# Kernel optimization log

Measured on AMD Instinct MI355X. Metric: run time of the kernel, lower is better.

## Reference

```python
import jax, jax.numpy as jnp
import numpy as np

B, M, N, K = 64, 1024, 1024, 128

def setup_inputs() -> dict:
    key = jax.random.key(0)
    k1, k2, k3 = jax.random.split(key, 3)
    # int8 operands (stored as int32 per spec; values fit in int8 range)
    a = jax.random.randint(k1, (B, M, K), 0, 127, dtype=jnp.int32)
    b = jax.random.randint(k2, (B, N, K), 0, 127, dtype=jnp.int32)  # S8N: N-major, matmul uses b^T
    alpha = jax.random.uniform(k3, (1,), dtype=jnp.float32) * 0.01
    return {"a": a, "b": b, "alpha": alpha}

def reference(a, b, alpha):
    acc = jnp.einsum('bmk,bnk->bmn', a, b)  # int32 accumulator
    # fused dequant epilogue: scale by alpha, cast to fp16
    return (alpha[0] * acc.astype(jnp.float32)).astype(jnp.float16)
```

## Files before the change

### kernel.cpp

```cpp
#include <hip/hip_runtime.h>


#define Mdim 1024
#define Ndim 1024
#define Kdim 128
#define TILE 128
#define LDS_STRIDE 144

using int32x4 = __attribute__((ext_vector_type(4))) int;
using floatx4 = __attribute__((ext_vector_type(4))) float;

__device__ __forceinline__ unsigned pack8(int32x4 v) {
    return (unsigned)(v.x & 255) | ((unsigned)(v.y & 255) << 8)
         | ((unsigned)(v.z & 255) << 16) | ((unsigned)(v.w & 255) << 24);
}

__global__ __launch_bounds__(256)
void bmm_s8_kernel(const int* __restrict__ A, const int* __restrict__ Bm,
                   const float* __restrict__ alpha_p, float* __restrict__ out)
{
    __shared__ unsigned char As[TILE * LDS_STRIDE];
    __shared__ unsigned char Bs[2][TILE * LDS_STRIDE];

    const int t      = threadIdx.x;
    const int z      = blockIdx.x;
    const int m_tile = blockIdx.y;
    const int m0     = m_tile * TILE;

    const int* __restrict__ Ab = A  + (size_t)z * Mdim * Kdim + (size_t)m0 * Kdim;
    const int* __restrict__ Bb = Bm + (size_t)z * Ndim * Kdim;

    const int lane = t & 63;
    const int wave = t >> 6;

    const int s_row  = (t + 0) >> 5;
    (void)s_row;

    {
        int32x4 areg[16], breg[16];
#pragma unroll
        for (int j = 0; j < 16; ++j) {
            const int f    = t + 256 * j;
            const int row  = f >> 5;
            const int colb = (f & 31) * 4;
            areg[j] = *(const int32x4*)(Ab + (size_t)row * Kdim + colb);
            breg[j] = *(const int32x4*)(Bb + (size_t)row * Kdim + colb);
        }
#pragma unroll
        for (int j = 0; j < 16; ++j) {
            const int f    = t + 256 * j;
            const int row  = f >> 5;
            const int colb = (f & 31) * 4;
            *(unsigned*)(&As[row * LDS_STRIDE + colb])    = pack8(areg[j]);
            *(unsigned*)(&Bs[0][row * LDS_STRIDE + colb]) = pack8(breg[j]);
        }
    }
    __syncthreads();

    const float alpha = alpha_p[0];
    const int wm   = (wave >> 1) * 64;
    const int wn   = (wave & 1) * 64;
    const int lrow = lane & 15;
    const int koff = (lane >> 4) * 16;
    const int cm   = lane & 15;
    const int cn   = (lane >> 4) * 4;
    float* __restrict__ Ob = out + (size_t)z * Mdim * Ndim;

#pragma unroll 1
    for (int ni = 0; ni < 8; ++ni) {
        const int buf = ni & 1;

        int32x4 breg[16];
        if (ni < 7) {
            const int* __restrict__ Bt = Bb + (size_t)(ni + 1) * TILE * Kdim;
#pragma unroll
            for (int j = 0; j < 16; ++j) {
                const int f    = t + 256 * j;
                const int row  = f >> 5;
                const int colb = (f & 31) * 4;
                breg[j] = *(const int32x4*)(Bt + (size_t)row * Kdim + colb);
            }
        }

        int32x4 acc[4][4];
#pragma unroll
        for (int mt = 0; mt < 4; ++mt)
#pragma unroll
            for (int nt = 0; nt < 4; ++nt)
                acc[mt][nt] = (int32x4){0, 0, 0, 0};

#pragma unroll
        for (int ks = 0; ks < 2; ++ks) {
            int32x4 af[4], bf[4];
#pragma unroll
            for (int mt = 0; mt < 4; ++mt)
                af[mt] = *(const int32x4*)(&As[(wm + mt * 16 + lrow) * LDS_STRIDE + ks * 64 + koff]);
#pragma unroll
            for (int nt = 0; nt < 4; ++nt)
                bf[nt] = *(const int32x4*)(&Bs[buf][(wn + nt * 16 + lrow) * LDS_STRIDE + ks * 64 + koff]);
#pragma unroll
            for (int mt = 0; mt < 4; ++mt)
#pragma unroll
                for (int nt = 0; nt < 4; ++nt)
                    acc[mt][nt] = __builtin_amdgcn_mfma_i32_16x16x64_i8(
                        bf[nt], af[mt], acc[mt][nt], 0, 0, 0);
        }

#pragma unroll
        for (int mt = 0; mt < 4; ++mt) {
            const size_t rowbase = (size_t)(m0 + wm + mt * 16 + cm) * Ndim;
#pragma unroll
            for (int nt = 0; nt < 4; ++nt) {
                const int col = ni * TILE + wn + nt * 16 + cn;
                floatx4 v;
                v.x = alpha * (float)acc[mt][nt][0];
                v.y = alpha * (float)acc[mt][nt][1];
                v.z = alpha * (float)acc[mt][nt][2];
                v.w = alpha * (float)acc[mt][nt][3];
                *(floatx4*)(Ob + rowbase + col) = v;
            }
        }

        if (ni < 7) {
#pragma unroll
            for (int j = 0; j < 16; ++j) {
                const int f    = t + 256 * j;
                const int row  = f >> 5;
                const int colb = (f & 31) * 4;
                *(unsigned*)(&Bs[buf ^ 1][row * LDS_STRIDE + colb]) = pack8(breg[j]);
            }
        }
        __syncthreads();
    }
}

extern "C" void kernel_launch(void* const* d_in, const int* in_sizes, int n_in,
                              void* d_out, int out_size, void* d_ws, size_t ws_size,
                              hipStream_t stream) {
    const int*   a     = (const int*)d_in[0];
    const int*   b     = (const int*)d_in[1];
    const float* alpha = (const float*)d_in[2];
    float*       out   = (float*)d_out;

    const int batch = in_sizes[0] / (Mdim * Kdim);
    dim3 grid(batch, Mdim / TILE);
    bmm_s8_kernel<<<grid, 256, 0, stream>>>(a, b, alpha, out);
}
```

Baseline: 346.8 us.

## Give each wave a private B slice so the per-tile barrier can go

The block's B tile is now split into 32-column slices. Each wave loads, packs and stores only its own slice into LDS, and reads back only that slice. This removes the cross-wave dependency on the double-buffered B tile, so the __syncthreads at the end of every N-tile iteration is dropped. The per-wave output tile changes from 64x64 to 128x32, which means more A fragment reads from LDS per wave and fewer B fragment reads. Correctness now depends on ordering LDS writes and reads within a single wave.

```diff
diff --git a/kernel.cpp b/kernel.cpp
--- a/kernel.cpp
+++ b/kernel.cpp
@@ -22,19 +22,16 @@
     __shared__ unsigned char As[TILE * LDS_STRIDE];
     __shared__ unsigned char Bs[2][TILE * LDS_STRIDE];
 
-    const int t      = threadIdx.x;
-    const int z      = blockIdx.x;
-    const int m_tile = blockIdx.y;
-    const int m0     = m_tile * TILE;
+    const int t  = threadIdx.x;
+    const int z  = blockIdx.x;
+    const int m0 = blockIdx.y * TILE;
 
     const int* __restrict__ Ab = A  + (size_t)z * Mdim * Kdim + (size_t)m0 * Kdim;
     const int* __restrict__ Bb = Bm + (size_t)z * Ndim * Kdim;
 
     const int lane = t & 63;
     const int wave = t >> 6;
-
-    const int s_row  = (t + 0) >> 5;
-    (void)s_row;
+    const int wn   = wave * 32;
 
     {
         int32x4 areg[16], breg[16];
@@ -44,22 +41,32 @@
             const int row  = f >> 5;
             const int colb = (f & 31) * 4;
             areg[j] = *(const int32x4*)(Ab + (size_t)row * Kdim + colb);
-            breg[j] = *(const int32x4*)(Bb + (size_t)row * Kdim + colb);
+        }
+#pragma unroll
+        for (int j = 0; j < 16; ++j) {
+            const int f    = lane + 64 * j;
+            const int rl   = f >> 5;
+            const int colb = (f & 31) * 4;
+            breg[j] = *(const int32x4*)(Bb + (size_t)(wn + rl) * Kdim + colb);
         }
 #pragma unroll
         for (int j = 0; j < 16; ++j) {
             const int f    = t + 256 * j;
             const int row  = f >> 5;
             const int colb = (f & 31) * 4;
-            *(unsigned*)(&As[row * LDS_STRIDE + colb])    = pack8(areg[j]);
-            *(unsigned*)(&Bs[0][row * LDS_STRIDE + colb]) = pack8(breg[j]);
+            *(unsigned*)(&As[row * LDS_STRIDE + colb]) = pack8(areg[j]);
+        }
+#pragma unroll
+        for (int j = 0; j < 16; ++j) {
+            const int f    = lane + 64 * j;
+            const int rl   = f >> 5;
+            const int colb = (f & 31) * 4;
+            *(unsigned*)(&Bs[0][(wn + rl) * LDS_STRIDE + colb]) = pack8(breg[j]);
         }
     }
     __syncthreads();
 
     const float alpha = alpha_p[0];
-    const int wm   = (wave >> 1) * 64;
-    const int wn   = (wave & 1) * 64;
     const int lrow = lane & 15;
     const int koff = (lane >> 4) * 16;
     const int cm   = lane & 15;
@@ -75,42 +82,42 @@
             const int* __restrict__ Bt = Bb + (size_t)(ni + 1) * TILE * Kdim;
 #pragma unroll
             for (int j = 0; j < 16; ++j) {
-                const int f    = t + 256 * j;
-                const int row  = f >> 5;
+                const int f    = lane + 64 * j;
+                const int rl   = f >> 5;
                 const int colb = (f & 31) * 4;
-                breg[j] = *(const int32x4*)(Bt + (size_t)row * Kdim + colb);
+                breg[j] = *(const int32x4*)(Bt + (size_t)(wn + rl) * Kdim + colb);
             }
         }
 
-        int32x4 acc[4][4];
+        int32x4 acc[8][2];
 #pragma unroll
-        for (int mt = 0; mt < 4; ++mt)
+        for (int mt = 0; mt < 8; ++mt)
 #pragma unroll
-            for (int nt = 0; nt < 4; ++nt)
+            for (int nt = 0; nt < 2; ++nt)
                 acc[mt][nt] = (int32x4){0, 0, 0, 0};
 
 #pragma unroll
         for (int ks = 0; ks < 2; ++ks) {
-            int32x4 af[4], bf[4];
+            int32x4 af[8], bf[2];
 #pragma unroll
-            for (int mt = 0; mt < 4; ++mt)
-                af[mt] = *(const int32x4*)(&As[(wm + mt * 16 + lrow) * LDS_STRIDE + ks * 64 + koff]);
+            for (int mt = 0; mt < 8; ++mt)
+                af[mt] = *(const int32x4*)(&As[(mt * 16 + lrow) * LDS_STRIDE + ks * 64 + koff]);
 #pragma unroll
-            for (int nt = 0; nt < 4; ++nt)
+            for (int nt = 0; nt < 2; ++nt)
                 bf[nt] = *(const int32x4*)(&Bs[buf][(wn + nt * 16 + lrow) * LDS_STRIDE + ks * 64 + koff]);
 #pragma unroll
-            for (int mt = 0; mt < 4; ++mt)
+            for (int mt = 0; mt < 8; ++mt)
 #pragma unroll
-                for (int nt = 0; nt < 4; ++nt)
+                for (int nt = 0; nt < 2; ++nt)
                     acc[mt][nt] = __builtin_amdgcn_mfma_i32_16x16x64_i8(
                         bf[nt], af[mt], acc[mt][nt], 0, 0, 0);
         }
 
 #pragma unroll
-        for (int mt = 0; mt < 4; ++mt) {
-            const size_t rowbase = (size_t)(m0 + wm + mt * 16 + cm) * Ndim;
+        for (int mt = 0; mt < 8; ++mt) {
+            const size_t rowbase = (size_t)(m0 + mt * 16 + cm) * Ndim;
 #pragma unroll
-            for (int nt = 0; nt < 4; ++nt) {
+            for (int nt = 0; nt < 2; ++nt) {
                 const int col = ni * TILE + wn + nt * 16 + cn;
                 floatx4 v;
                 v.x = alpha * (float)acc[mt][nt][0];
@@ -124,13 +131,12 @@
         if (ni < 7) {
 #pragma unroll
             for (int j = 0; j < 16; ++j) {
-                const int f    = t + 256 * j;
-                const int row  = f >> 5;
+                const int f    = lane + 64 * j;
+                const int rl   = f >> 5;
                 const int colb = (f & 31) * 4;
-                *(unsigned*)(&Bs[buf ^ 1][row * LDS_STRIDE + colb]) = pack8(breg[j]);
+                *(unsigned*)(&Bs[buf ^ 1][(wn + rl) * LDS_STRIDE + colb]) = pack8(breg[j]);
             }
         }
-        __syncthreads();
     }
 }
 
```

Result: no change. 343.9 us (-0.8%).

## Keep full B matrix in LDS and stream A strips directly into registers

Applied to the files above, without the earlier changes.

Each 512-thread block now stages the whole 1024x128 int8 B matrix of its batch in a swizzled LDS buffer and walks 256 rows of A in 16-row strips. A fragments are loaded straight from global memory into registers and prefetched one strip ahead, instead of going through LDS. Each wave computes a 16x128 output strip per iteration. This removes the A LDS staging and the per-tile B reload, so B is read from global memory less often. The cost is 128KB of LDS per block, which limits occupancy, plus a barrier per strip that is not needed.

```diff
diff --git a/kernel.cpp b/kernel.cpp
--- a/kernel.cpp
+++ b/kernel.cpp
@@ -4,8 +4,9 @@
 #define Mdim 1024
 #define Ndim 1024
 #define Kdim 128
-#define TILE 128
-#define LDS_STRIDE 144
+#define NROWS 16
+#define NSTRIPS 16
+#define BSTRIDE 128
 
 using int32x4 = __attribute__((ext_vector_type(4))) int;
 using floatx4 = __attribute__((ext_vector_type(4))) float;
@@ -15,121 +16,104 @@
          | ((unsigned)(v.z & 255) << 16) | ((unsigned)(v.w & 255) << 24);
 }
 
-__global__ __launch_bounds__(256)
+__device__ __forceinline__ int swz(int byte_off) {
+    return byte_off ^ (((byte_off >> 7) & 7) << 4);
+}
+
+__global__ __launch_bounds__(512, 2)
 void bmm_s8_kernel(const int* __restrict__ A, const int* __restrict__ Bm,
                    const float* __restrict__ alpha_p, float* __restrict__ out)
 {
-    __shared__ unsigned char As[TILE * LDS_STRIDE];
-    __shared__ unsigned char Bs[2][TILE * LDS_STRIDE];
+    __shared__ unsigned char Bs[1024 * BSTRIDE];
 
-    const int t      = threadIdx.x;
-    const int z      = blockIdx.x;
-    const int m_tile = blockIdx.y;
-    const int m0     = m_tile * TILE;
-
-    const int* __restrict__ Ab = A  + (size_t)z * Mdim * Kdim + (size_t)m0 * Kdim;
-    const int* __restrict__ Bb = Bm + (size_t)z * Ndim * Kdim;
-
+    const int t    = threadIdx.x;
+    const int z    = blockIdx.x;
+    const int q    = blockIdx.y;
     const int lane = t & 63;
     const int wave = t >> 6;
+    const int wn   = wave * 128;
 
-    const int s_row  = (t + 0) >> 5;
-    (void)s_row;
+    const int* __restrict__ Ab = A  + (size_t)z * Mdim * Kdim + (size_t)(q * 256) * Kdim;
+    const int* __restrict__ Bb = Bm + (size_t)z * Ndim * Kdim;
+    float* __restrict__ Ob     = out + (size_t)z * Mdim * Ndim + (size_t)(q * 256) * Ndim;
 
-    {
-        int32x4 areg[16], breg[16];
+    const int r = lane & 15;
+    const int g = lane >> 4;
+
+    int32x4 araw[8];
+#pragma unroll
+    for (int k = 0; k < 8; ++k) {
+        const int ks = k >> 2, i = k & 3;
+        araw[k] = *(const int32x4*)(Ab + (size_t)r * Kdim + ks * 64 + g * 16 + i * 4);
+    }
+
+#pragma unroll 1
+    for (int rr = 0; rr < 4; ++rr) {
+        int32x4 breg[16];
 #pragma unroll
         for (int j = 0; j < 16; ++j) {
-            const int f    = t + 256 * j;
+            const int f    = t + 512 * (rr * 16 + j);
             const int row  = f >> 5;
             const int colb = (f & 31) * 4;
-            areg[j] = *(const int32x4*)(Ab + (size_t)row * Kdim + colb);
             breg[j] = *(const int32x4*)(Bb + (size_t)row * Kdim + colb);
         }
 #pragma unroll
         for (int j = 0; j < 16; ++j) {
-            const int f    = t + 256 * j;
+            const int f    = t + 512 * (rr * 16 + j);
             const int row  = f >> 5;
             const int colb = (f & 31) * 4;
-            *(unsigned*)(&As[row * LDS_STRIDE + colb])    = pack8(areg[j]);
-            *(unsigned*)(&Bs[0][row * LDS_STRIDE + colb]) = pack8(breg[j]);
+            *(unsigned*)(&Bs[swz(row * BSTRIDE + colb)]) = pack8(breg[j]);
         }
     }
     __syncthreads();
 
     const float alpha = alpha_p[0];
-    const int wm   = (wave >> 1) * 64;
-    const int wn   = (wave & 1) * 64;
-    const int lrow = lane & 15;
-    const int koff = (lane >> 4) * 16;
-    const int cm   = lane & 15;
-    const int cn   = (lane >> 4) * 4;
-    float* __restrict__ Ob = out + (size_t)z * Mdim * Ndim;
+    const int cm = lane & 15;
+    const int cn = (lane >> 4) * 4;
 
 #pragma unroll 1
-    for (int ni = 0; ni < 8; ++ni) {
-        const int buf = ni & 1;
+    for (int s = 0; s < NSTRIPS; ++s) {
+        int32x4 af[2];
+#pragma unroll
+        for (int ks = 0; ks < 2; ++ks)
+            af[ks] = (int32x4){ (int)pack8(araw[ks * 4 + 0]), (int)pack8(araw[ks * 4 + 1]),
+                                (int)pack8(araw[ks * 4 + 2]), (int)pack8(araw[ks * 4 + 3]) };
 
-        int32x4 breg[16];
-        if (ni < 7) {
-            const int* __restrict__ Bt = Bb + (size_t)(ni + 1) * TILE * Kdim;
+        if (s + 1 < NSTRIPS) {
+            const int* __restrict__ An = Ab + (size_t)((s + 1) * NROWS) * Kdim;
 #pragma unroll
-            for (int j = 0; j < 16; ++j) {
-                const int f    = t + 256 * j;
-                const int row  = f >> 5;
-                const int colb = (f & 31) * 4;
-                breg[j] = *(const int32x4*)(Bt + (size_t)row * Kdim + colb);
+            for (int k = 0; k < 8; ++k) {
+                const int ks = k >> 2, i = k & 3;
+                araw[k] = *(const int32x4*)(An + (size_t)r * Kdim + ks * 64 + g * 16 + i * 4);
             }
         }
 
-        int32x4 acc[4][4];
+        int32x4 acc[8];
 #pragma unroll
-        for (int mt = 0; mt < 4; ++mt)
-#pragma unroll
-            for (int nt = 0; nt < 4; ++nt)
-                acc[mt][nt] = (int32x4){0, 0, 0, 0};
+        for (int nt = 0; nt < 8; ++nt)
+            acc[nt] = (int32x4){0, 0, 0, 0};
 
 #pragma unroll
         for (int ks = 0; ks < 2; ++ks) {
-            int32x4 af[4], bf[4];
 #pragma unroll
-            for (int mt = 0; mt < 4; ++mt)
-                af[mt] = *(const int32x4*)(&As[(wm + mt * 16 + lrow) * LDS_STRIDE + ks * 64 + koff]);
-#pragma unroll
-            for (int nt = 0; nt < 4; ++nt)
-                bf[nt] = *(const int32x4*)(&Bs[buf][(wn + nt * 16 + lrow) * LDS_STRIDE + ks * 64 + koff]);
-#pragma unroll
-            for (int mt = 0; mt < 4; ++mt)
-#pragma unroll
-                for (int nt = 0; nt < 4; ++nt)
-                    acc[mt][nt] = __builtin_amdgcn_mfma_i32_16x16x64_i8(
-                        bf[nt], af[mt], acc[mt][nt], 0, 0, 0);
-        }
-
-#pragma unroll
-        for (int mt = 0; mt < 4; ++mt) {
-            const size_t rowbase = (size_t)(m0 + wm + mt * 16 + cm) * Ndim;
-#pragma unroll
-            for (int nt = 0; nt < 4; ++nt) {
-                const int col = ni * TILE + wn + nt * 16 + cn;
-                floatx4 v;
-                v.x = alpha * (float)acc[mt][nt][0];
-                v.y = alpha * (float)acc[mt][nt][1];
-                v.z = alpha * (float)acc[mt][nt][2];
-                v.w = alpha * (float)acc[mt][nt][3];
-                *(floatx4*)(Ob + rowbase + col) = v;
+            for (int nt = 0; nt < 8; ++nt) {
+                const int row = wn + nt * 16 + r;
+                int32x4 bf = *(const int32x4*)(&Bs[swz(row * BSTRIDE + ks * 64 + g * 16)]);
+                acc[nt] = __builtin_amdgcn_mfma_i32_16x16x64_i8(bf, af[ks], acc[nt], 0, 0, 0);
             }
         }
 
-        if (ni < 7) {
+        const size_t rowbase = (size_t)(s * NROWS + cm) * Ndim + wn;
 #pragma unroll
-            for (int j = 0; j < 16; ++j) {
-                const int f    = t + 256 * j;
-                const int row  = f >> 5;
-                const int colb = (f & 31) * 4;
-                *(unsigned*)(&Bs[buf ^ 1][row * LDS_STRIDE + colb]) = pack8(breg[j]);
-            }
+        for (int nt = 0; nt < 8; ++nt) {
+            floatx4 v;
+            v.x = alpha * (float)acc[nt][0];
+            v.y = alpha * (float)acc[nt][1];
+            v.z = alpha * (float)acc[nt][2];
+            v.w = alpha * (float)acc[nt][3];
+            *(floatx4*)(Ob + rowbase + nt * 16 + cn) = v;
         }
+
         __syncthreads();
     }
 }
@@ -143,6 +127,6 @@
     float*       out   = (float*)d_out;
 
     const int batch = in_sizes[0] / (Mdim * Kdim);
-    dim3 grid(batch, Mdim / TILE);
-    bmm_s8_kernel<<<grid, 256, 0, stream>>>(a, b, alpha, out);
+    dim3 grid(batch, Mdim / (NROWS * NSTRIPS));
+    bmm_s8_kernel<<<grid, 512, 0, stream>>>(a, b, alpha, out);
 }
```

Measured after the change: 343.5 us. About the same (-1.0%).
